# Kernel optimization log

Measured on AMD Instinct MI355X. Metric: run time of the kernel, lower is better.

Reference implementation:

```python
import jax, jax.numpy as jnp
import numpy as np

B, J, T = 64, 24, 2048
FOOT_IDX = (7, 8, 10, 11)
LAMBDA_VEL = 0.2
LAMBDA_FOOT = 0.1
CONTACT_THRESH = 0.05


def setup_inputs() -> dict:
    key = jax.random.key(0)
    k1, k2, k3 = jax.random.split(key, 3)
    pred = jax.random.normal(k1, (B, J, 6, T), dtype=jnp.float32)
    target = jax.random.normal(k2, (B, J, 6, T), dtype=jnp.float32)
    joint_positions = jax.random.normal(k3, (B, J, 3, T), dtype=jnp.float32)
    return {"pred": pred, "target": target, "joint_positions": joint_positions}


def _foot_contact_loss(joint_positions):
    # joint_positions: [B, J, 3, T]
    foot_pos = joint_positions[:, jnp.array(FOOT_IDX), :, :]        # [B, F, 3, T]
    foot_height = foot_pos[:, :, 1, :]                              # [B, F, T]
    contact_w = jax.nn.sigmoid((CONTACT_THRESH - foot_height) * 20.0)
    foot_vel = foot_pos[:, :, :, 1:] - foot_pos[:, :, :, :-1]       # [B, F, 3, T-1]
    foot_vel_xz = foot_vel[:, :, jnp.array([0, 2]), :]              # [B, F, 2, T-1]
    cw_vel = (contact_w[:, :, 1:] + contact_w[:, :, :-1]) * 0.5     # [B, F, T-1]
    loss = (foot_vel_xz ** 2).sum(axis=2) * cw_vel                  # [B, F, T-1]
    num_contacts = cw_vel.sum() + 1e-8
    return loss.sum() / num_contacts


def reference(pred, target, joint_positions):
    # Reconstruction MSE on 6D rotations
    recon = jnp.mean((pred - target) ** 2)
    # First-order velocity loss over frames (last axis)
    dp = pred[:, :, :, 1:] - pred[:, :, :, :-1]
    dt = target[:, :, :, 1:] - target[:, :, :, :-1]
    vel = jnp.mean((dp - dt) ** 2)
    # Foot contact (anti-sliding) loss
    foot = _foot_contact_loss(joint_positions)
    total = recon + LAMBDA_VEL * vel + LAMBDA_FOOT * foot
    return total
```

## Files before the change

kernel.cpp:

```cpp
#include <hip/hip_runtime.h>

#define BB 64
#define JJ 24
#define TT 2048
#define NELEM (BB*JJ*6*TT)
#define NVEL  ((long long)BB*JJ*6*(TT-1))
#define FOOT_BLOCKS 256
#define RGRID 2048
#define RTHREADS (RGRID*256)
#define NBLK (RGRID + FOOT_BLOCKS)

__device__ __forceinline__ void block_reduce2(float& a, float& b) {
    #pragma unroll
    for (int off = 32; off > 0; off >>= 1) {
        a += __shfl_down(a, off);
        b += __shfl_down(b, off);
    }
    __shared__ float sa[4], sb[4];
    const int lane = threadIdx.x & 63;
    const int wid  = threadIdx.x >> 6;
    if (lane == 0) { sa[wid] = a; sb[wid] = b; }
    __syncthreads();
    if (threadIdx.x == 0) {
        for (int w = 1; w < 4; ++w) { a += sa[w]; b += sb[w]; }
    }
}

__device__ __forceinline__ float sigm(float y) {
    return 1.f / (1.f + __expf(-(0.05f - y) * 20.f));
}

__global__ __launch_bounds__(256) void fused_kernel(
        const float* __restrict__ pred, const float* __restrict__ targ,
        const float* __restrict__ jp, double2* __restrict__ parts) {

    if (blockIdx.x < FOOT_BLOCKS) {
        const int FI[4] = {7, 8, 10, 11};
        const int bf = blockIdx.x;
        const int b  = bf >> 2;
        const int j  = FI[bf & 3];
        const float* __restrict__ xrow = jp + ((size_t)(b * JJ + j) * 3) * TT;
        const float* __restrict__ yrow = xrow + TT;
        const float* __restrict__ zrow = xrow + 2 * TT;
        const float4* __restrict__ x4 = reinterpret_cast<const float4*>(xrow);
        const float4* __restrict__ y4 = reinterpret_cast<const float4*>(yrow);
        const float4* __restrict__ z4 = reinterpret_cast<const float4*>(zrow);

        float lsum = 0.f, csum = 0.f;
        #pragma unroll
        for (int cc = 0; cc < 2; ++cc) {
            const int c = threadIdx.x + cc * 256;
            const float4 xv = x4[c], yv = y4[c], zv = z4[c];
            float x0 = 0.f, y0 = 0.f, z0 = 0.f;
            if (c > 0) { x0 = xrow[4*c-1]; y0 = yrow[4*c-1]; z0 = zrow[4*c-1]; }
            const float w0 = sigm(y0),  w1 = sigm(yv.x), w2 = sigm(yv.y),
                        w3 = sigm(yv.z), w4 = sigm(yv.w);
            auto term = [&](float x1, float xp, float z1, float zp,
                            float wa, float wb) {
                const float cw = 0.5f * (wa + wb);
                const float vx = x1 - xp, vz = z1 - zp;
                lsum += (vx * vx + vz * vz) * cw;
                csum += cw;
            };
            if (c > 0) term(xv.x, x0, zv.x, z0, w1, w0);
            term(xv.y, xv.x, zv.y, zv.x, w2, w1);
            term(xv.z, xv.y, zv.z, zv.y, w3, w2);
            term(xv.w, xv.z, zv.w, zv.z, w4, w3);
        }
        block_reduce2(lsum, csum);
        if (threadIdx.x == 0)
            parts[blockIdx.x] = make_double2((double)lsum, (double)csum);
    } else {
        const float4* __restrict__ pred4 = reinterpret_cast<const float4*>(pred);
        const float4* __restrict__ targ4 = reinterpret_cast<const float4*>(targ);
        const int tid = (blockIdx.x - FOOT_BLOCKS) * 256 + threadIdx.x;
        float recon = 0.f, vel = 0.f;

        auto proc = [&](const float4& p, const float4& g, int i) {
            const float d0 = p.x - g.x, d1 = p.y - g.y,
                        d2 = p.z - g.z, d3 = p.w - g.w;
            recon += d0*d0 + d1*d1 + d2*d2 + d3*d3;
            const float e01 = d1 - d0, e12 = d2 - d1, e23 = d3 - d2;
            vel += e01*e01 + e12*e12 + e23*e23;
            const float dprev = __shfl_up(d3, 1);
            const int e = i * 4;
            if (e & (TT - 1)) {
                float dm1 = dprev;
                if ((threadIdx.x & 63) == 0)
                    dm1 = pred[e - 1] - targ[e - 1];
                const float b0 = d0 - dm1;
                vel += b0 * b0;
            }
        };

        #pragma unroll
        for (int grp = 0; grp < 3; ++grp) {
            const int i0 = tid + grp * 3 * RTHREADS;
            const float4 P0 = pred4[i0];
            const float4 G0 = targ4[i0];
            const float4 P1 = pred4[i0 + RTHREADS];
            const float4 G1 = targ4[i0 + RTHREADS];
            const float4 P2 = pred4[i0 + 2 * RTHREADS];
            const float4 G2 = targ4[i0 + 2 * RTHREADS];
            proc(P0, G0, i0);
            proc(P1, G1, i0 + RTHREADS);
            proc(P2, G2, i0 + 2 * RTHREADS);
        }
        block_reduce2(recon, vel);
        if (threadIdx.x == 0)
            parts[blockIdx.x] = make_double2((double)recon, (double)vel);
    }
}

__global__ __launch_bounds__(64) void finalize_kernel(
        const double2* __restrict__ parts, float* __restrict__ out) {
    double foot_l = 0.0, foot_c = 0.0, recon = 0.0, vel = 0.0;
    for (int i = threadIdx.x; i < NBLK; i += 64) {
        const double2 v = parts[i];
        if (i < FOOT_BLOCKS) { foot_l += v.x; foot_c += v.y; }
        else                 { recon  += v.x; vel    += v.y; }
    }
    #pragma unroll
    for (int off = 32; off > 0; off >>= 1) {
        recon  += __shfl_down(recon,  off);
        vel    += __shfl_down(vel,    off);
        foot_l += __shfl_down(foot_l, off);
        foot_c += __shfl_down(foot_c, off);
    }
    if (threadIdx.x == 0) {
        const double r = recon / (double)NELEM;
        const double v = vel   / (double)NVEL;
        const double f = foot_l / (foot_c + 1e-8);
        out[0] = (float)(r + 0.2 * v + 0.1 * f);
    }
}

extern "C" void kernel_launch(void* const* d_in, const int* in_sizes, int n_in,
                              void* d_out, int out_size, void* d_ws, size_t ws_size,
                              hipStream_t stream) {
    const float* pred = (const float*)d_in[0];
    const float* targ = (const float*)d_in[1];
    const float* jp   = (const float*)d_in[2];
    float* out     = (float*)d_out;
    double2* parts = (double2*)d_ws;

    fused_kernel<<<NBLK, 256, 0, stream>>>(pred, targ, jp, parts);
    finalize_kernel<<<1, 64, 0, stream>>>(parts, out);
}
```

Before: 199.0 us.

## Fold finalize into main kernel via last-block atomic and use contiguous per-thread chunks

The separate finalize kernel is replaced by a last-block-done pattern: each block bumps an atomic counter after writing its partial, and the final block reduces all partials and writes the output. A memset of the counter is added before launch. The recon/velocity path now gives each thread 16 contiguous elements, loaded as four float4 per input, so most of the velocity differences stay in registers. This removes the wavefront shuffles and the grid-strided loop, and the grid grows to 4608 reduction blocks. The aim is to cut one kernel launch, but it adds a memset, an atomic per block, and strided rather than coalesced float4 accesses within a wavefront.

```diff
diff --git a/kernel.cpp b/kernel.cpp
--- a/kernel.cpp
+++ b/kernel.cpp
@@ -6,11 +6,10 @@
 #define NELEM (BB*JJ*6*TT)
 #define NVEL  ((long long)BB*JJ*6*(TT-1))
 #define FOOT_BLOCKS 256
-#define RGRID 2048
-#define RTHREADS (RGRID*256)
-#define NBLK (RGRID + FOOT_BLOCKS)
+#define RBLOCKS 4608
+#define NBLK (FOOT_BLOCKS + RBLOCKS)
 
-__device__ __forceinline__ void block_reduce2(float& a, float& b) {
+__device__ __forceinline__ void block_reduce2f(float& a, float& b) {
     #pragma unroll
     for (int off = 32; off > 0; off >>= 1) {
         a += __shfl_down(a, off);
@@ -32,7 +31,8 @@
 
 __global__ __launch_bounds__(256) void fused_kernel(
         const float* __restrict__ pred, const float* __restrict__ targ,
-        const float* __restrict__ jp, double2* __restrict__ parts) {
+        const float* __restrict__ jp, unsigned* __restrict__ counter,
+        double2* __restrict__ parts, float* __restrict__ out) {
 
     if (blockIdx.x < FOOT_BLOCKS) {
         const int FI[4] = {7, 8, 10, 11};
@@ -67,70 +67,76 @@
             term(xv.z, xv.y, zv.z, zv.y, w3, w2);
             term(xv.w, xv.z, zv.w, zv.z, w4, w3);
         }
-        block_reduce2(lsum, csum);
+        block_reduce2f(lsum, csum);
         if (threadIdx.x == 0)
             parts[blockIdx.x] = make_double2((double)lsum, (double)csum);
     } else {
+        const int tid = (blockIdx.x - FOOT_BLOCKS) * 256 + threadIdx.x;
+        const int c4  = tid * 4;
+        const int e0  = tid * 16;
         const float4* __restrict__ pred4 = reinterpret_cast<const float4*>(pred);
         const float4* __restrict__ targ4 = reinterpret_cast<const float4*>(targ);
-        const int tid = (blockIdx.x - FOOT_BLOCKS) * 256 + threadIdx.x;
+
+        float4 P[4], G[4];
+        #pragma unroll
+        for (int k = 0; k < 4; ++k) { P[k] = pred4[c4 + k]; G[k] = targ4[c4 + k]; }
+        float pm = 0.f, gm = 0.f;
+        const int t0 = e0 & (TT - 1);
+        if (t0 != 0) { pm = pred[e0 - 1]; gm = targ[e0 - 1]; }
+
+        float d[16];
+        #pragma unroll
+        for (int k = 0; k < 4; ++k) {
+            d[4*k+0] = P[k].x - G[k].x;
+            d[4*k+1] = P[k].y - G[k].y;
+            d[4*k+2] = P[k].z - G[k].z;
+            d[4*k+3] = P[k].w - G[k].w;
+        }
         float recon = 0.f, vel = 0.f;
+        #pragma unroll
+        for (int k = 0; k < 16; ++k) recon += d[k] * d[k];
+        #pragma unroll
+        for (int k = 1; k < 16; ++k) { const float e = d[k] - d[k-1]; vel += e*e; }
+        if (t0 != 0) { const float e = d[0] - (pm - gm); vel += e * e; }
 
-        auto proc = [&](const float4& p, const float4& g, int i) {
-            const float d0 = p.x - g.x, d1 = p.y - g.y,
-                        d2 = p.z - g.z, d3 = p.w - g.w;
-            recon += d0*d0 + d1*d1 + d2*d2 + d3*d3;
-            const float e01 = d1 - d0, e12 = d2 - d1, e23 = d3 - d2;
-            vel += e01*e01 + e12*e12 + e23*e23;
-            const float dprev = __shfl_up(d3, 1);
-            const int e = i * 4;
-            if (e & (TT - 1)) {
-                float dm1 = dprev;
-                if ((threadIdx.x & 63) == 0)
-                    dm1 = pred[e - 1] - targ[e - 1];
-                const float b0 = d0 - dm1;
-                vel += b0 * b0;
-            }
-        };
-
-        #pragma unroll
-        for (int grp = 0; grp < 3; ++grp) {
-            const int i0 = tid + grp * 3 * RTHREADS;
-            const float4 P0 = pred4[i0];
-            const float4 G0 = targ4[i0];
-            const float4 P1 = pred4[i0 + RTHREADS];
-            const float4 G1 = targ4[i0 + RTHREADS];
-            const float4 P2 = pred4[i0 + 2 * RTHREADS];
-            const float4 G2 = targ4[i0 + 2 * RTHREADS];
-            proc(P0, G0, i0);
-            proc(P1, G1, i0 + RTHREADS);
-            proc(P2, G2, i0 + 2 * RTHREADS);
-        }
-        block_reduce2(recon, vel);
+        block_reduce2f(recon, vel);
         if (threadIdx.x == 0)
             parts[blockIdx.x] = make_double2((double)recon, (double)vel);
     }
-}
 
-__global__ __launch_bounds__(64) void finalize_kernel(
-        const double2* __restrict__ parts, float* __restrict__ out) {
-    double foot_l = 0.0, foot_c = 0.0, recon = 0.0, vel = 0.0;
-    for (int i = threadIdx.x; i < NBLK; i += 64) {
+    __shared__ bool amLast;
+    if (threadIdx.x == 0) {
+        __threadfence();
+        amLast = (atomicAdd(counter, 1u) == (unsigned)(NBLK - 1));
+    }
+    __syncthreads();
+    if (!amLast) return;
+    __threadfence();
+
+    double fl = 0.0, fc = 0.0, rc = 0.0, vl = 0.0;
+    for (int i = threadIdx.x; i < NBLK; i += 256) {
         const double2 v = parts[i];
-        if (i < FOOT_BLOCKS) { foot_l += v.x; foot_c += v.y; }
-        else                 { recon  += v.x; vel    += v.y; }
+        if (i < FOOT_BLOCKS) { fl += v.x; fc += v.y; }
+        else                 { rc += v.x; vl += v.y; }
     }
     #pragma unroll
     for (int off = 32; off > 0; off >>= 1) {
-        recon  += __shfl_down(recon,  off);
-        vel    += __shfl_down(vel,    off);
-        foot_l += __shfl_down(foot_l, off);
-        foot_c += __shfl_down(foot_c, off);
+        rc += __shfl_down(rc, off);
+        vl += __shfl_down(vl, off);
+        fl += __shfl_down(fl, off);
+        fc += __shfl_down(fc, off);
     }
+    __shared__ double s4[4][4];
+    const int lane = threadIdx.x & 63, wid = threadIdx.x >> 6;
+    if (lane == 0) { s4[wid][0]=rc; s4[wid][1]=vl; s4[wid][2]=fl; s4[wid][3]=fc; }
+    __syncthreads();
     if (threadIdx.x == 0) {
-        const double r = recon / (double)NELEM;
-        const double v = vel   / (double)NVEL;
-        const double f = foot_l / (foot_c + 1e-8);
+        for (int w = 1; w < 4; ++w) {
+            rc += s4[w][0]; vl += s4[w][1]; fl += s4[w][2]; fc += s4[w][3];
+        }
+        const double r = rc / (double)NELEM;
+        const double v = vl / (double)NVEL;
+        const double f = fl / (fc + 1e-8);
         out[0] = (float)(r + 0.2 * v + 0.1 * f);
     }
 }
@@ -141,9 +147,10 @@
     const float* pred = (const float*)d_in[0];
     const float* targ = (const float*)d_in[1];
     const float* jp   = (const float*)d_in[2];
-    float* out     = (float*)d_out;
-    double2* parts = (double2*)d_ws;
+    float* out        = (float*)d_out;
+    unsigned* counter = (unsigned*)d_ws;
+    double2* parts    = (double2*)((char*)d_ws + 256);
 
-    fused_kernel<<<NBLK, 256, 0, stream>>>(pred, targ, jp, parts);
-    finalize_kernel<<<1, 64, 0, stream>>>(parts, out);
+    hipMemsetAsync(d_ws, 0, 4, stream);
+    fused_kernel<<<NBLK, 256, 0, stream>>>(pred, targ, jp, counter, parts, out);
 }
```

New measurement: 410.0 us. 106% more time.
